# Optimization experiments

Measured on AMD Instinct MI355X. Metric: run time of the kernel, lower is better.

## Reference

```python
import jax, jax.numpy as jnp
import numpy as np

C = 256          # hidden_channel
FFN = 1024       # ffn_channel
NCLS = 10
BS, N = 2, 2048  # batch, num_proposals
GRID = 180.0     # grid_size/out_size_factor
EPS_OT = 10.0
IPOT_ITERS = 100


def _ln(x, g, b, eps=1e-5):
    mu = jnp.mean(x, axis=-1, keepdims=True)
    var = jnp.var(x, axis=-1, keepdims=True)
    return (x - mu) * jax.lax.rsqrt(var + eps) * g + b


def setup_inputs() -> dict:
    key = jax.random.key(0)
    ks = jax.random.split(key, 32)
    s = 0.02
    inp = {
        "pts_query_feat": jax.random.normal(ks[0], (BS, C, N), jnp.float32),
        "pts_query_pos": jax.random.uniform(ks[1], (BS, N, 2), jnp.float32) * GRID,
        "img_query_feat": jax.random.normal(ks[2], (BS, C, N), jnp.float32),
        "img_query_pos": jax.random.uniform(ks[3], (BS, N, 2), jnp.float32) * GRID,
        "pts_cls": jax.random.normal(ks[4], (BS, NCLS, N), jnp.float32),
        "img_cls": jax.random.normal(ks[5], (BS, NCLS, N), jnp.float32),
        # pts/img 1x1-conv projections
        "Wp": jax.random.normal(ks[6], (C, C), jnp.float32) * s,
        "bp": jnp.zeros((C,), jnp.float32),
        "Wi": jax.random.normal(ks[7], (C, C), jnp.float32) * s,
        "bi": jnp.zeros((C,), jnp.float32),
        # learned position embeddings (2 -> C)
        "Wqp": jax.random.normal(ks[8], (C, 2), jnp.float32) * s,
        "bqp": jnp.zeros((C,), jnp.float32),
        "Wkp": jax.random.normal(ks[9], (C, 2), jnp.float32) * s,
        "bkp": jnp.zeros((C,), jnp.float32),
        # out_projection: Linear(2C, C) + LayerNorm(C)
        "Wout": jax.random.normal(ks[10], (C, 2 * C), jnp.float32) * s,
        "bout": jnp.zeros((C,), jnp.float32),
        "g_out": jnp.ones((C,), jnp.float32),
        "beta_out": jnp.zeros((C,), jnp.float32),
        # ffn
        "Wf1": jax.random.normal(ks[11], (FFN, C), jnp.float32) * s,
        "bf1": jnp.zeros((FFN,), jnp.float32),
        "Wf2": jax.random.normal(ks[12], (C, FFN), jnp.float32) * s,
        "bf2": jnp.zeros((C,), jnp.float32),
        # final LayerNorm
        "g_ln": jnp.ones((C,), jnp.float32),
        "b_ln": jnp.zeros((C,), jnp.float32),
        # prediction head: 1x1 conv C -> 2 (center)
        "Wpred": jax.random.normal(ks[13], (2, C), jnp.float32) * s,
        "bpred": jnp.zeros((2,), jnp.float32),
    }
    return inp


def ipot(pts_feat, img_feat, pts_cls, img_cls, cost):
    # pts_feat/img_feat: [bs, C, N]; pts_cls/img_cls: [bs, N]; cost: [bs, N, N]
    n = pts_cls.shape[1]
    b0 = jnp.ones_like(pts_cls) / n
    G = jnp.exp(-cost / EPS_OT)
    res0 = jnp.ones_like(G)

    def step(carry, _):
        b, res = carry
        Q = jnp.maximum(G * res, 1e-6)
        a = pts_cls / (jnp.einsum("bnm,bm->bn", Q, b) + 1e-6)
        b = img_cls / (jnp.einsum("bnm,bn->bm", Q, a) + 1e-6)
        # diag_embed(a) @ Q @ diag_embed(b) == a[:,:,None] * Q * b[:,None,:]
        res = a[:, :, None] * Q * b[:, None, :]
        return (b, res), None

    (b, res), _ = jax.lax.scan(step, (b0, res0), None, length=IPOT_ITERS)
    # F.normalize(res, dim=2, p=1); res is nonnegative
    res = res / jnp.maximum(jnp.sum(jnp.abs(res), axis=2, keepdims=True), 1e-12)
    img_att = jnp.einsum("bnm,bcm->bcn", res, img_feat)  # [bs, C, N]
    return jnp.concatenate([pts_feat, img_att], axis=1)   # [bs, 2C, N]


def reference(pts_query_feat, pts_query_pos, img_query_feat, img_query_pos,
              pts_cls, img_cls,
              Wp, bp, Wi, bi, Wqp, bqp, Wkp, bkp,
              Wout, bout, g_out, beta_out,
              Wf1, bf1, Wf2, bf2, g_ln, b_ln, Wpred, bpred):
    # channel projections (1x1 conv over N)
    pf = jnp.einsum("oc,bcn->bon", Wp, pts_query_feat) + bp[:, None]
    imf = jnp.einsum("oc,bcn->bon", Wi, img_query_feat) + bi[:, None]
    # learned positional embeddings: [bs,N,2] -> [bs,C,N]
    pf = pf + jnp.einsum("cd,bnd->bcn", Wqp, pts_query_pos) + bqp[:, None]
    imf = imf + jnp.einsum("cd,bnd->bcn", Wkp, img_query_pos) + bkp[:, None]
    # detached per-proposal confidences
    pcls = jax.lax.stop_gradient(jnp.max(jax.nn.sigmoid(pts_cls), axis=1))
    icls = jax.lax.stop_gradient(jnp.max(jax.nn.sigmoid(img_cls), axis=1))
    # pairwise L2 cost [bs, N, N]
    diff = pts_query_pos[:, :, None, :] - img_query_pos[:, None, :, :]
    cost = jnp.sqrt(jnp.sum(diff * diff, axis=-1))
    feat = ipot(pf, imf, pcls, icls, cost)            # [bs, 2C, N]
    x = jnp.swapaxes(feat, 1, 2)                      # [bs, N, 2C]
    x = _ln(x @ Wout.T + bout, g_out, beta_out)       # out_projection
    ffn = jax.nn.relu(x @ Wf1.T + bf1) @ Wf2.T + bf2  # ffn
    x = ffn + x                                       # ffn(x) + dropout(x), eval mode
    x = jnp.swapaxes(_ln(x, g_ln, b_ln), 1, 2)        # [bs, C, N]
    center = jnp.einsum("oc,bcn->bon", Wpred, x) + bpred[:, None]
    center = center + jnp.swapaxes(pts_query_pos, 1, 2)  # [bs, 2, N]
    new_pos = jnp.swapaxes(jax.lax.stop_gradient(center), 1, 2)  # [bs, N, 2]
    return (x, new_pos, center)
```

## Files before the change

### kernel.cpp

```cpp
#include <hip/hip_runtime.h>
#include <hip/hip_bf16.h>

#define N2   2048
#define CH   256
#define FFNC 1024

typedef unsigned short ushort_t;
typedef unsigned int   uint_t;

#define OFF_QB     0u
#define OFF_IMFT   4194304u
#define OFF_CPART  5242880u
#define OFF_PCLS   7340032u
#define OFF_ICLS   7344128u
#define OFF_BVEC   7348224u
#define OFF_AVEC   7352320u
#define OFF_WOUTT  7356416u
#define OFF_WF1T   7487488u
#define OFF_WF2T   7749632u

__device__ __forceinline__ float bf2f(uint_t u) {
    return __uint_as_float(u << 16);
}
__device__ __forceinline__ ushort_t f2bf(float f) {
    __hip_bfloat16 h = __float2bfloat16(f);
    ushort_t u;
    __builtin_memcpy(&u, &h, 2);
    return u;
}

__device__ __forceinline__ void blockReduce2(float& x, float& y, float* sred) {
    #pragma unroll
    for (int off = 32; off; off >>= 1) {
        x += __shfl_xor(x, off);
        y += __shfl_xor(y, off);
    }
    const int wave = threadIdx.x >> 6, lane = threadIdx.x & 63;
    if (lane == 0) { sred[wave] = x; sred[4 + wave] = y; }
    __syncthreads();
    x = sred[0] + sred[1] + sred[2] + sred[3];
    y = sred[4] + sred[5] + sred[6] + sred[7];
    __syncthreads();
}

__global__ void __launch_bounds__(256) cls_max_k(
    const float* __restrict__ pc, const float* __restrict__ ic,
    float* __restrict__ pcls, float* __restrict__ icls) {
    const int g = blockIdx.x * 256 + threadIdx.x;
    const int b = g >> 11, n = g & 2047;
    float m1 = -1e30f, m2 = -1e30f;
    #pragma unroll
    for (int k = 0; k < 10; ++k) {
        const float v1 = pc[((size_t)b * 10 + k) * N2 + n];
        const float v2 = ic[((size_t)b * 10 + k) * N2 + n];
        m1 = fmaxf(m1, 1.f / (1.f + __expf(-v1)));
        m2 = fmaxf(m2, 1.f / (1.f + __expf(-v2)));
    }
    pcls[g] = m1; icls[g] = m2;
}

__global__ void __launch_bounds__(256) transpose_k(
    const float* __restrict__ in, float* __restrict__ out, int R, int C) {
    __shared__ float t[32][33];
    const int nct = C >> 5;
    const int bx = blockIdx.x % nct, by = blockIdx.x / nct;
    const int c0 = bx * 32, r0 = by * 32;
    const int tx = threadIdx.x & 31, ty = threadIdx.x >> 5;
    #pragma unroll
    for (int i = 0; i < 4; ++i) {
        const int r = ty + i * 8;
        t[r][tx] = in[(size_t)(r0 + r) * C + c0 + tx];
    }
    __syncthreads();
    #pragma unroll
    for (int i = 0; i < 4; ++i) {
        const int r = ty + i * 8;
        out[(size_t)(c0 + r) * R + r0 + tx] = t[tx][r];
    }
}

__global__ void __launch_bounds__(256) proj_rows(
    const float* __restrict__ F, const float* __restrict__ WT,
    const float* __restrict__ bias, const float* __restrict__ Wpos,
    const float* __restrict__ bpos, const float* __restrict__ pos,
    float* __restrict__ outb) {
    const int b = blockIdx.x >> 8;
    const int n0 = (blockIdx.x & 255) * 8;
    const int tid = threadIdx.x;
    __shared__ float s_x[8][256];
    for (int idx = tid; idx < 2048; idx += 256) {
        const int r = idx & 7, c = idx >> 3;
        s_x[r][c] = F[((size_t)b * CH + c) * N2 + n0 + r];
    }
    __syncthreads();
    float acc[8] = {0, 0, 0, 0, 0, 0, 0, 0};
    for (int c = 0; c < 256; ++c) {
        const float w = WT[(size_t)c * CH + tid];
        #pragma unroll
        for (int r = 0; r < 8; ++r) acc[r] += s_x[r][c] * w;
    }
    const float badd = bias[tid] + bpos[tid];
    const float w0 = Wpos[tid * 2 + 0], w1 = Wpos[tid * 2 + 1];
    #pragma unroll
    for (int r = 0; r < 8; ++r) {
        const int n = n0 + r;
        const float p0 = pos[((size_t)b * N2 + n) * 2 + 0];
        const float p1 = pos[((size_t)b * N2 + n) * 2 + 1];
        outb[((size_t)b * N2 + n) * CH + tid] = acc[r] + badd + w0 * p0 + w1 * p1;
    }
}


__device__ __forceinline__ void load_cols8(const float* ipos, int batch, int tid,
                                           float* ixr, float* iyr) {
    const float4* ip4 = (const float4*)(ipos + (size_t)batch * (N2 * 2));
    #pragma unroll
    for (int m = 0; m < 4; ++m) {
        const float4 v = ip4[4 * tid + m];
        ixr[2 * m + 0] = v.x; iyr[2 * m + 0] = v.y;
        ixr[2 * m + 1] = v.z; iyr[2 * m + 1] = v.w;
    }
}

__device__ __forceinline__ void unpack8(const uint4 v, float* q) {
    q[0] = bf2f(v.x & 0xffffu); q[1] = bf2f(v.x >> 16);
    q[2] = bf2f(v.y & 0xffffu); q[3] = bf2f(v.y >> 16);
    q[4] = bf2f(v.z & 0xffffu); q[5] = bf2f(v.z >> 16);
    q[6] = bf2f(v.w & 0xffffu); q[7] = bf2f(v.w >> 16);
}

__device__ __forceinline__ uint4 pack8(const float* q) {
    uint4 v;
    v.x = (uint_t)f2bf(q[0]) | ((uint_t)f2bf(q[1]) << 16);
    v.y = (uint_t)f2bf(q[2]) | ((uint_t)f2bf(q[3]) << 16);
    v.z = (uint_t)f2bf(q[4]) | ((uint_t)f2bf(q[5]) << 16);
    v.w = (uint_t)f2bf(q[6]) | ((uint_t)f2bf(q[7]) << 16);
    return v;
}

__global__ void __launch_bounds__(256, 4) ipot_init_k(
    ushort_t* __restrict__ Q, const float* __restrict__ ppos, const float* __restrict__ ipos,
    const float* __restrict__ pcls, float* __restrict__ avec, float* __restrict__ cpart) {
    const int blk = blockIdx.x;
    const int batch = blk >> 9;
    const int p = blk & 511;
    const int r0 = p * 4;
    const int tid = threadIdx.x, wave = tid >> 6, lane = tid & 63;
    __shared__ float s_tot[4][4];

    float ixr[8], iyr[8];
    load_cols8(ipos, batch, tid, ixr, iyr);
    float px[4], py[4], pcl4[4];
    #pragma unroll
    for (int j = 0; j < 4; ++j) {
        px[j] = ppos[((size_t)batch * N2 + r0 + j) * 2 + 0];
        py[j] = ppos[((size_t)batch * N2 + r0 + j) * 2 + 1];
        pcl4[j] = pcls[batch * N2 + r0 + j];
    }
    ushort_t* Qb = Q + (size_t)batch * N2 * N2;
    float cs[8] = {0, 0, 0, 0, 0, 0, 0, 0};

    float qn[4][8];
    float rd[4];
    #pragma unroll
    for (int jj = 0; jj < 4; ++jj) {
        rd[jj] = 0.f;
        #pragma unroll
        for (int k = 0; k < 8; ++k) {
            const float dx = px[jj] - ixr[k], dy = py[jj] - iyr[k];
            const float v = fmaxf(__expf(-0.1f * sqrtf(dx * dx + dy * dy)), 1e-6f);
            qn[jj][k] = bf2f(f2bf(v));
            rd[jj] += qn[jj][k];
        }
        ((uint4*)(Qb + (size_t)(r0 + jj) * N2))[tid] = pack8(qn[jj]);
    }
    #pragma unroll
    for (int off = 32; off; off >>= 1) {
        #pragma unroll
        for (int jj = 0; jj < 4; ++jj) rd[jj] += __shfl_xor(rd[jj], off);
    }
    if (lane == 0) {
        #pragma unroll
        for (int jj = 0; jj < 4; ++jj) s_tot[wave][jj] = rd[jj];
    }
    __syncthreads();
    #pragma unroll
    for (int jj = 0; jj < 4; ++jj) {
        const float tot = s_tot[0][jj] + s_tot[1][jj] + s_tot[2][jj] + s_tot[3][jj];
        const float a = pcl4[jj] / (tot * (1.f / 2048.f) + 1e-6f);
        if (tid == 0) avec[batch * N2 + r0 + jj] = a;
        #pragma unroll
        for (int k = 0; k < 8; ++k) cs[k] += a * qn[jj][k];
    }
    float4* cp4 = (float4*)(cpart + ((size_t)batch * 512 + p) * N2);
    float4 l, h4;
    l.x = cs[0]; l.y = cs[1]; l.z = cs[2]; l.w = cs[3];
    h4.x = cs[4]; h4.y = cs[5]; h4.z = cs[6]; h4.w = cs[7];
    cp4[2 * tid] = l; cp4[2 * tid + 1] = h4;
}

__global__ void __launch_bounds__(256) ipot_red_k(
    const float* __restrict__ cpart, const float* __restrict__ icls,
    float* __restrict__ bvec) {
    const int b = blockIdx.x >> 5;
    const int c0 = (blockIdx.x & 31) * 64;
    const int tid = threadIdx.x;
    const int c = tid & 63, pg = tid >> 6;
    __shared__ float s_part[4][64];
    const float* cpb = cpart + (size_t)b * 512 * N2 + c0 + c;
    float s = 0.f;
    #pragma unroll 8
    for (int k = 0; k < 128; ++k) s += cpb[(size_t)(pg + 4 * k) * N2];
    s_part[pg][c] = s;
    __syncthreads();
    if (tid < 64) {
        const float tot = s_part[0][tid] + s_part[1][tid] + s_part[2][tid] + s_part[3][tid];
        bvec[b * N2 + c0 + tid] = icls[b * N2 + c0 + tid] / (tot + 1e-6f);
    }
}

__global__ void __launch_bounds__(256, 4) ipot_ur_k(
    ushort_t* __restrict__ Q, const float* __restrict__ ppos, const float* __restrict__ ipos,
    const float* __restrict__ pcls, const float* __restrict__ bvec,
    float* __restrict__ avec, float* __restrict__ cpart) {
    const int blk = blockIdx.x;
    const int batch = blk >> 9;
    const int p = blk & 511;
    const int r0 = p * 4;
    const int tid = threadIdx.x, wave = tid >> 6, lane = tid & 63;
    __shared__ float s_tot[4][4];

    float ixr[8], iyr[8];
    load_cols8(ipos, batch, tid, ixr, iyr);
    float bb[8];
    {
        const float4* bv4 = (const float4*)(bvec + (size_t)batch * N2);
        const float4 l = bv4[2 * tid], h4 = bv4[2 * tid + 1];
        bb[0] = l.x; bb[1] = l.y; bb[2] = l.z; bb[3] = l.w;
        bb[4] = h4.x; bb[5] = h4.y; bb[6] = h4.z; bb[7] = h4.w;
    }
    float px[4], py[4], pcl4[4], a_cur[4];
    #pragma unroll
    for (int j = 0; j < 4; ++j) {
        px[j] = ppos[((size_t)batch * N2 + r0 + j) * 2 + 0];
        py[j] = ppos[((size_t)batch * N2 + r0 + j) * 2 + 1];
        pcl4[j] = pcls[batch * N2 + r0 + j];
        a_cur[j] = avec[batch * N2 + r0 + j];
    }
    ushort_t* Qb = Q + (size_t)batch * N2 * N2;
    float cs[8] = {0, 0, 0, 0, 0, 0, 0, 0};

    float qn[4][8];
    float rd[4];
    #pragma unroll
    for (int jj = 0; jj < 4; ++jj) {
        uint4* row4 = (uint4*)(Qb + (size_t)(r0 + jj) * N2);
        float qv[8];
        unpack8(row4[tid], qv);
        rd[jj] = 0.f;
        const float a = a_cur[jj];
        #pragma unroll
        for (int k = 0; k < 8; ++k) {
            const float dx = px[jj] - ixr[k], dy = py[jj] - iyr[k];
            const float G = __expf(-0.1f * sqrtf(dx * dx + dy * dy));
            const float v = fmaxf(G * ((a * qv[k]) * bb[k]), 1e-6f);
            qn[jj][k] = bf2f(f2bf(v));
            rd[jj] += qn[jj][k] * bb[k];
        }
        row4[tid] = pack8(qn[jj]);
    }
    #pragma unroll
    for (int off = 32; off; off >>= 1) {
        #pragma unroll
        for (int jj = 0; jj < 4; ++jj) rd[jj] += __shfl_xor(rd[jj], off);
    }
    if (lane == 0) {
        #pragma unroll
        for (int jj = 0; jj < 4; ++jj) s_tot[wave][jj] = rd[jj];
    }
    __syncthreads();
    #pragma unroll
    for (int jj = 0; jj < 4; ++jj) {
        const float tot = s_tot[0][jj] + s_tot[1][jj] + s_tot[2][jj] + s_tot[3][jj];
        const float a = pcl4[jj] / (tot + 1e-6f);
        if (tid == 0) avec[batch * N2 + r0 + jj] = a;
        #pragma unroll
        for (int k = 0; k < 8; ++k) cs[k] += a * qn[jj][k];
    }
    float4* cp4 = (float4*)(cpart + ((size_t)batch * 512 + p) * N2);
    float4 l, h4;
    l.x = cs[0]; l.y = cs[1]; l.z = cs[2]; l.w = cs[3];
    h4.x = cs[4]; h4.y = cs[5]; h4.z = cs[6]; h4.w = cs[7];
    cp4[2 * tid] = l; cp4[2 * tid + 1] = h4;
}

__global__ void __launch_bounds__(256, 4) ipot_fin_k(
    ushort_t* __restrict__ Q, const float* __restrict__ pcls,
    const float* __restrict__ bvec, const float* __restrict__ avec) {
    const int blk = blockIdx.x;
    const int batch = blk >> 9;
    const int p = blk & 511;
    const int r0 = p * 4;
    const int tid = threadIdx.x, wave = tid >> 6, lane = tid & 63;
    __shared__ float s_tot[4][4];

    float bb[8];
    {
        const float4* bv4 = (const float4*)(bvec + (size_t)batch * N2);
        const float4 l = bv4[2 * tid], h4 = bv4[2 * tid + 1];
        bb[0] = l.x; bb[1] = l.y; bb[2] = l.z; bb[3] = l.w;
        bb[4] = h4.x; bb[5] = h4.y; bb[6] = h4.z; bb[7] = h4.w;
    }
    float a4[4];
    #pragma unroll
    for (int j = 0; j < 4; ++j) a4[j] = avec[batch * N2 + r0 + j];
    ushort_t* Qb = Q + (size_t)batch * N2 * N2;

    float vv[4][8];
    float rs[4];
    #pragma unroll
    for (int jj = 0; jj < 4; ++jj) {
        uint4* row4 = (uint4*)(Qb + (size_t)(r0 + jj) * N2);
        float qv[8];
        unpack8(row4[tid], qv);
        rs[jj] = 0.f;
        const float a = a4[jj];
        #pragma unroll
        for (int k = 0; k < 8; ++k) {
            const float v = (a * qv[k]) * bb[k];
            vv[jj][k] = v;
            rs[jj] += v;
        }
    }
    #pragma unroll
    for (int off = 32; off; off >>= 1) {
        #pragma unroll
        for (int jj = 0; jj < 4; ++jj) rs[jj] += __shfl_xor(rs[jj], off);
    }
    if (lane == 0) {
        #pragma unroll
        for (int jj = 0; jj < 4; ++jj) s_tot[wave][jj] = rs[jj];
    }
    __syncthreads();
    #pragma unroll
    for (int jj = 0; jj < 4; ++jj) {
        const float tot = s_tot[0][jj] + s_tot[1][jj] + s_tot[2][jj] + s_tot[3][jj];
        const float sc = 1.f / fmaxf(tot, 1e-12f);
        float o[8];
        #pragma unroll
        for (int k = 0; k < 8; ++k) o[k] = vv[jj][k] * sc;
        ((uint4*)(Qb + (size_t)(r0 + jj) * N2))[tid] = pack8(o);
    }
}

__global__ void __launch_bounds__(256) att_zero_k(float* __restrict__ att) {
    const int idx = blockIdx.x * 256 + threadIdx.x;
    float4 z; z.x = 0.f; z.y = 0.f; z.z = 0.f; z.w = 0.f;
    ((float4*)att)[idx] = z;
}

__global__ void __launch_bounds__(256, 4) att_gemm(
    const ushort_t* __restrict__ R, const float* __restrict__ V, float* __restrict__ att) {
    const int bid = blockIdx.x;
    const int nt = bid & 31, ct = (bid >> 5) & 3, ks = (bid >> 7) & 3, b = bid >> 9;
    const int n0 = nt * 64, c0 = ct * 64, k00 = ks * 512;
    __shared__ float sRT[16][68];
    __shared__ float sV[16][68];
    const int tid = threadIdx.x;
    const int ny = tid & 15, cx = tid >> 4;
    float acc[4][4] = {};
    const ushort_t* Rb = R + (size_t)b * N2 * N2;
    const float* Vb = V + (size_t)b * N2 * CH;
    const int snl = tid & 63, skk0 = (tid >> 6) * 4;
    for (int k0 = k00; k0 < k00 + 512; k0 += 16) {
        {
            const uint2 v = *(const uint2*)&Rb[(size_t)(n0 + snl) * N2 + k0 + skk0];
            sRT[skk0 + 0][snl] = bf2f(v.x & 0xffffu);
            sRT[skk0 + 1][snl] = bf2f(v.x >> 16);
            sRT[skk0 + 2][snl] = bf2f(v.y & 0xffffu);
            sRT[skk0 + 3][snl] = bf2f(v.y >> 16);
        }
        for (int idx = tid; idx < 1024; idx += 256) {
            const int kk = idx >> 6, cl = idx & 63;
            sV[kk][cl] = Vb[(size_t)(k0 + kk) * CH + c0 + cl];
        }
        __syncthreads();
        #pragma unroll
        for (int kk = 0; kk < 16; ++kk) {
            const float4 av = *(const float4*)&sRT[kk][4 * ny];
            const float4 bv = *(const float4*)&sV[kk][4 * cx];
            acc[0][0] += av.x * bv.x; acc[0][1] += av.x * bv.y; acc[0][2] += av.x * bv.z; acc[0][3] += av.x * bv.w;
            acc[1][0] += av.y * bv.x; acc[1][1] += av.y * bv.y; acc[1][2] += av.y * bv.z; acc[1][3] += av.y * bv.w;
            acc[2][0] += av.z * bv.x; acc[2][1] += av.z * bv.y; acc[2][2] += av.z * bv.z; acc[2][3] += av.z * bv.w;
            acc[3][0] += av.w * bv.x; acc[3][1] += av.w * bv.y; acc[3][2] += av.w * bv.z; acc[3][3] += av.w * bv.w;
        }
        __syncthreads();
    }
    #pragma unroll
    for (int i = 0; i < 4; ++i)
        #pragma unroll
        for (int j = 0; j < 4; ++j)
            atomicAdd(&att[((size_t)b * N2 + n0 + 4 * ny + i) * CH + c0 + 4 * cx + j], acc[i][j]);
}

__global__ void __launch_bounds__(256) outproj_k(
    const float* __restrict__ pf, const float* __restrict__ att,
    const float* __restrict__ WoutT,
    const float* __restrict__ bout, const float* __restrict__ g,
    const float* __restrict__ be, float* __restrict__ y) {
    const int b = blockIdx.x >> 8;
    const int n0 = (blockIdx.x & 255) * 8;
    const int tid = threadIdx.x;
    __shared__ float s_x[8][512];
    __shared__ float sred[8];
    for (int idx = tid; idx < 2048; idx += 256) {
        const int k = idx & 255, r = idx >> 8;
        s_x[r][k] = pf[((size_t)b * N2 + n0 + r) * CH + k];
        s_x[r][256 + k] = att[((size_t)b * N2 + n0 + r) * CH + k];
    }
    __syncthreads();
    float acc[8] = {0, 0, 0, 0, 0, 0, 0, 0};
    for (int k = 0; k < 512; ++k) {
        const float w = WoutT[(size_t)k * CH + tid];
        #pragma unroll
        for (int r = 0; r < 8; ++r) acc[r] += s_x[r][k] * w;
    }
    const float bo = bout[tid], gg = g[tid], bb = be[tid];
    #pragma unroll
    for (int r = 0; r < 8; ++r) {
        const float v = acc[r] + bo;
        float s1 = v, s2 = v * v;
        blockReduce2(s1, s2, sred);
        const float mu = s1 * (1.f / 256.f);
        const float var = s2 * (1.f / 256.f) - mu * mu;
        y[((size_t)b * N2 + n0 + r) * CH + tid] = (v - mu) * rsqrtf(var + 1e-5f) * gg + bb;
    }
}

__global__ void __launch_bounds__(256) ffn_k(
    const float* __restrict__ y, const float* __restrict__ Wf1T,
    const float* __restrict__ bf1, const float* __restrict__ Wf2T,
    const float* __restrict__ bf2, const float* __restrict__ gln,
    const float* __restrict__ bln, const float* __restrict__ Wpred,
    const float* __restrict__ bpred, const float* __restrict__ pos,
    float* __restrict__ y2, float* __restrict__ out1,
    float* __restrict__ out2) {
    const int b = blockIdx.x >> 8;
    const int n0 = (blockIdx.x & 255) * 8;
    const int tid = threadIdx.x;
    __shared__ float s_y[8][256];
    __shared__ float s_h[8][1024];
    __shared__ float sred[8];
    for (int idx = tid; idx < 2048; idx += 256) {
        const int c = idx & 255, r = idx >> 8;
        s_y[r][c] = y[((size_t)b * N2 + n0 + r) * CH + c];
    }
    __syncthreads();
    float acc[4][8] = {};
    for (int c = 0; c < 256; ++c) {
        float yv[8];
        #pragma unroll
        for (int r = 0; r < 8; ++r) yv[r] = s_y[r][c];
        #pragma unroll
        for (int fi = 0; fi < 4; ++fi) {
            const float w = Wf1T[(size_t)c * FFNC + fi * 256 + tid];
            #pragma unroll
            for (int r = 0; r < 8; ++r) acc[fi][r] += yv[r] * w;
        }
    }
    #pragma unroll
    for (int fi = 0; fi < 4; ++fi) {
        const int f = fi * 256 + tid;
        const float bb = bf1[f];
        #pragma unroll
        for (int r = 0; r < 8; ++r) s_h[r][f] = fmaxf(acc[fi][r] + bb, 0.f);
    }
    __syncthreads();
    float a2[8] = {0, 0, 0, 0, 0, 0, 0, 0};
    for (int f = 0; f < 1024; ++f) {
        const float w = Wf2T[(size_t)f * CH + tid];
        #pragma unroll
        for (int r = 0; r < 8; ++r) a2[r] += s_h[r][f] * w;
    }
    const float bfv = bf2[tid], gg = gln[tid], bb2 = bln[tid];
    const float wp0 = Wpred[tid], wp1 = Wpred[CH + tid];
    #pragma unroll
    for (int r = 0; r < 8; ++r) {
        const int n = n0 + r;
        const float v = a2[r] + bfv + s_y[r][tid];
        float s1 = v, s2 = v * v;
        blockReduce2(s1, s2, sred);
        const float mu = s1 * (1.f / 256.f);
        const float var = s2 * (1.f / 256.f) - mu * mu;
        const float xo = (v - mu) * rsqrtf(var + 1e-5f) * gg + bb2;
        y2[((size_t)b * N2 + n) * CH + tid] = xo;
        float d0 = wp0 * xo, d1 = wp1 * xo;
        blockReduce2(d0, d1, sred);
        if (tid == 0) {
            const float c0v = d0 + bpred[0] + pos[((size_t)b * N2 + n) * 2 + 0];
            const float c1v = d1 + bpred[1] + pos[((size_t)b * N2 + n) * 2 + 1];
            out2[((size_t)b * 2 + 0) * N2 + n] = c0v;
            out2[((size_t)b * 2 + 1) * N2 + n] = c1v;
            out1[((size_t)b * N2 + n) * 2 + 0] = c0v;
            out1[((size_t)b * N2 + n) * 2 + 1] = c1v;
        }
    }
}

__global__ void __launch_bounds__(256) out_x_k(
    const float* __restrict__ y2, float* __restrict__ out0) {
    __shared__ float t[32][33];
    const int bid = blockIdx.x;
    const int ct = bid & 7, nt = (bid >> 3) & 63, b = bid >> 9;
    const int tx = threadIdx.x & 31, ty = threadIdx.x >> 5;
    #pragma unroll
    for (int i = 0; i < 4; ++i) {
        const int r = ty + i * 8;
        t[r][tx] = y2[((size_t)b * N2 + nt * 32 + r) * CH + ct * 32 + tx];
    }
    __syncthreads();
    #pragma unroll
    for (int i = 0; i < 4; ++i) {
        const int r = ty + i * 8;
        out0[((size_t)b * CH + ct * 32 + r) * N2 + nt * 32 + tx] = t[tx][r];
    }
}

extern "C" void kernel_launch(void* const* d_in, const int* in_sizes, int n_in,
                              void* d_out, int out_size, void* d_ws, size_t ws_size,
                              hipStream_t stream) {
    const float* ptsf  = (const float*)d_in[0];
    const float* ppos  = (const float*)d_in[1];
    const float* imgf  = (const float*)d_in[2];
    const float* ipos  = (const float*)d_in[3];
    const float* pcin  = (const float*)d_in[4];
    const float* icin  = (const float*)d_in[5];
    const float* Wp    = (const float*)d_in[6];
    const float* bp    = (const float*)d_in[7];
    const float* Wi    = (const float*)d_in[8];
    const float* bi    = (const float*)d_in[9];
    const float* Wqp   = (const float*)d_in[10];
    const float* bqp   = (const float*)d_in[11];
    const float* Wkp   = (const float*)d_in[12];
    const float* bkp   = (const float*)d_in[13];
    const float* Wout  = (const float*)d_in[14];
    const float* bout  = (const float*)d_in[15];
    const float* gout  = (const float*)d_in[16];
    const float* beo   = (const float*)d_in[17];
    const float* Wf1   = (const float*)d_in[18];
    const float* bf1   = (const float*)d_in[19];
    const float* Wf2   = (const float*)d_in[20];
    const float* bf2   = (const float*)d_in[21];
    const float* gln   = (const float*)d_in[22];
    const float* bln   = (const float*)d_in[23];
    const float* Wpred = (const float*)d_in[24];
    const float* bpred = (const float*)d_in[25];

    float* ws    = (float*)d_ws;
    ushort_t* Qw = (ushort_t*)d_ws;
    float* imfT  = ws + OFF_IMFT;
    float* cpart = ws + OFF_CPART;
    float* att   = ws + OFF_CPART;
    float* WiT   = ws + OFF_CPART;
    float* pcls  = ws + OFF_PCLS;
    float* icls  = ws + OFF_ICLS;
    float* bvec  = ws + OFF_BVEC;
    float* avec  = ws + OFF_AVEC;
    float* WoutT = ws + OFF_WOUTT;
    float* Wf1T  = ws + OFF_WF1T;
    float* Wf2T  = ws + OFF_WF2T;
    float* pf    = ws + 0u;
    float* yb    = ws + 1048576u;
    float* y2    = ws + 2097152u;
    float* WpT   = ws + 3145728u;

    float* out0 = (float*)d_out;
    float* out1 = out0 + (size_t)2 * CH * N2;
    float* out2 = out1 + (size_t)2 * N2 * 2;

    cls_max_k<<<16, 256, 0, stream>>>(pcin, icin, pcls, icls);
    transpose_k<<<64, 256, 0, stream>>>(Wi, WiT, 256, 256);
    proj_rows<<<512, 256, 0, stream>>>(imgf, WiT, bi, Wkp, bkp, ipos, imfT);
    transpose_k<<<128, 256, 0, stream>>>(Wout, WoutT, 256, 512);
    transpose_k<<<256, 256, 0, stream>>>(Wf1, Wf1T, 1024, 256);
    transpose_k<<<256, 256, 0, stream>>>(Wf2, Wf2T, 256, 1024);

    ipot_init_k<<<1024, 256, 0, stream>>>(Qw, ppos, ipos, pcls, avec, cpart);
    for (int t = 1; t < 100; ++t) {
        ipot_red_k<<<64, 256, 0, stream>>>(cpart, icls, bvec);
        ipot_ur_k<<<1024, 256, 0, stream>>>(Qw, ppos, ipos, pcls, bvec, avec, cpart);
    }
    ipot_red_k<<<64, 256, 0, stream>>>(cpart, icls, bvec);
    ipot_fin_k<<<1024, 256, 0, stream>>>(Qw, pcls, bvec, avec);

    att_zero_k<<<1024, 256, 0, stream>>>(att);
    att_gemm<<<1024, 256, 0, stream>>>(Qw, imfT, att);

    transpose_k<<<64, 256, 0, stream>>>(Wp, WpT, 256, 256);
    proj_rows<<<512, 256, 0, stream>>>(ptsf, WpT, bp, Wqp, bqp, ppos, pf);
    outproj_k<<<512, 256, 0, stream>>>(pf, att, WoutT, bout, gout, beo, yb);
    ffn_k<<<512, 256, 0, stream>>>(yb, Wf1T, bf1, Wf2T, bf2, gln, bln,
                                   Wpred, bpred, ppos, y2, out1, out2);
    out_x_k<<<1024, 256, 0, stream>>>(y2, out0);
}
```

Before: 2.581 ms.

## Fuse IPOT column reduction into update kernel with inter-block flag barrier

Removes the separate column-reduction launch from each IPOT iteration. The first 256 blocks of the update kernel compute bvec and bump a global counter, while every block loads its Q tile and computes the G*a*q product before spinning on the flag. The partial-sum buffer is double-buffered so that reads and writes within an iteration do not collide. This cuts launch count roughly in half and overlaps Q loading with the reduction. The cost is a cross-block spin-wait that relies on the reducer blocks being scheduled, and a slow fallback path if the wait times out.

```diff
diff --git a/kernel.cpp b/kernel.cpp
--- a/kernel.cpp
+++ b/kernel.cpp
@@ -10,14 +10,16 @@
 
 #define OFF_QB     0u
 #define OFF_IMFT   4194304u
-#define OFF_CPART  5242880u
-#define OFF_PCLS   7340032u
-#define OFF_ICLS   7344128u
-#define OFF_BVEC   7348224u
-#define OFF_AVEC   7352320u
-#define OFF_WOUTT  7356416u
-#define OFF_WF1T   7487488u
-#define OFF_WF2T   7749632u
+#define OFF_CPART0 5242880u
+#define OFF_CPART1 7340032u
+#define OFF_PCLS   9437184u
+#define OFF_ICLS   9441280u
+#define OFF_BVEC   9445376u
+#define OFF_AVEC   9449472u
+#define OFF_FLAG   9453568u
+#define OFF_WOUTT  9457664u
+#define OFF_WF1T   9588736u
+#define OFF_WF2T   9850880u
 
 __device__ __forceinline__ float bf2f(uint_t u) {
     return __uint_as_float(u << 16);
@@ -140,7 +142,8 @@
 
 __global__ void __launch_bounds__(256, 4) ipot_init_k(
     ushort_t* __restrict__ Q, const float* __restrict__ ppos, const float* __restrict__ ipos,
-    const float* __restrict__ pcls, float* __restrict__ avec, float* __restrict__ cpart) {
+    const float* __restrict__ pcls, float* __restrict__ avec, float* __restrict__ cpartW,
+    uint_t* __restrict__ flag) {
     const int blk = blockIdx.x;
     const int batch = blk >> 9;
     const int p = blk & 511;
@@ -148,6 +151,9 @@
     const int tid = threadIdx.x, wave = tid >> 6, lane = tid & 63;
     __shared__ float s_tot[4][4];
 
+    if (blk == 0 && tid == 0)
+        __hip_atomic_store(flag, 0u, __ATOMIC_RELAXED, __HIP_MEMORY_SCOPE_AGENT);
+
     float ixr[8], iyr[8];
     load_cols8(ipos, batch, tid, ixr, iyr);
     float px[4], py[4], pcl4[4];
@@ -192,7 +198,7 @@
         #pragma unroll
         for (int k = 0; k < 8; ++k) cs[k] += a * qn[jj][k];
     }
-    float4* cp4 = (float4*)(cpart + ((size_t)batch * 512 + p) * N2);
+    float4* cp4 = (float4*)(cpartW + ((size_t)batch * 512 + p) * N2);
     float4 l, h4;
     l.x = cs[0]; l.y = cs[1]; l.z = cs[2]; l.w = cs[3];
     h4.x = cs[4]; h4.y = cs[5]; h4.z = cs[6]; h4.w = cs[7];
@@ -221,24 +227,46 @@
 
 __global__ void __launch_bounds__(256, 4) ipot_ur_k(
     ushort_t* __restrict__ Q, const float* __restrict__ ppos, const float* __restrict__ ipos,
-    const float* __restrict__ pcls, const float* __restrict__ bvec,
-    float* __restrict__ avec, float* __restrict__ cpart) {
+    const float* __restrict__ pcls, const float* __restrict__ icls,
+    float* __restrict__ avec, const float* __restrict__ cpartR,
+    float* __restrict__ cpartW, float* __restrict__ bvec,
+    uint_t* __restrict__ flag, int t) {
     const int blk = blockIdx.x;
     const int batch = blk >> 9;
     const int p = blk & 511;
     const int r0 = p * 4;
     const int tid = threadIdx.x, wave = tid >> 6, lane = tid & 63;
     __shared__ float s_tot[4][4];
+    __shared__ float s_red[16][17];
+    __shared__ int s_fb;
+
+    if (blk < 256) {
+        const int pb = blk >> 7;
+        const int c0 = (blk & 127) * 16;
+        const int cl = tid & 15, pg = tid >> 4;
+        const float* cpb = cpartR + (size_t)pb * 512 * N2 + c0 + cl;
+        float s = 0.f;
+        #pragma unroll 8
+        for (int k = 0; k < 32; ++k) s += cpb[(size_t)(pg + 16 * k) * N2];
+        s_red[pg][cl] = s;
+        __syncthreads();
+        if (tid < 16) {
+            float tot = 0.f;
+            #pragma unroll
+            for (int g2 = 0; g2 < 16; ++g2) tot += s_red[g2][tid];
+            const float bv = icls[pb * N2 + c0 + tid] / (tot + 1e-6f);
+            __hip_atomic_store(&bvec[pb * N2 + c0 + tid], bv,
+                               __ATOMIC_RELAXED, __HIP_MEMORY_SCOPE_AGENT);
+        }
+        __syncthreads();
+        if (tid == 0) {
+            __threadfence();
+            __hip_atomic_fetch_add(flag, 1u, __ATOMIC_RELEASE, __HIP_MEMORY_SCOPE_AGENT);
+        }
+    }
 
     float ixr[8], iyr[8];
     load_cols8(ipos, batch, tid, ixr, iyr);
-    float bb[8];
-    {
-        const float4* bv4 = (const float4*)(bvec + (size_t)batch * N2);
-        const float4 l = bv4[2 * tid], h4 = bv4[2 * tid + 1];
-        bb[0] = l.x; bb[1] = l.y; bb[2] = l.z; bb[3] = l.w;
-        bb[4] = h4.x; bb[5] = h4.y; bb[6] = h4.z; bb[7] = h4.w;
-    }
     float px[4], py[4], pcl4[4], a_cur[4];
     #pragma unroll
     for (int j = 0; j < 4; ++j) {
@@ -248,26 +276,61 @@
         a_cur[j] = avec[batch * N2 + r0 + j];
     }
     ushort_t* Qb = Q + (size_t)batch * N2 * N2;
-    float cs[8] = {0, 0, 0, 0, 0, 0, 0, 0};
-
-    float qn[4][8];
-    float rd[4];
+    float w[4][8];
     #pragma unroll
     for (int jj = 0; jj < 4; ++jj) {
-        uint4* row4 = (uint4*)(Qb + (size_t)(r0 + jj) * N2);
         float qv[8];
-        unpack8(row4[tid], qv);
-        rd[jj] = 0.f;
+        unpack8(((const uint4*)(Qb + (size_t)(r0 + jj) * N2))[tid], qv);
         const float a = a_cur[jj];
         #pragma unroll
         for (int k = 0; k < 8; ++k) {
             const float dx = px[jj] - ixr[k], dy = py[jj] - iyr[k];
             const float G = __expf(-0.1f * sqrtf(dx * dx + dy * dy));
-            const float v = fmaxf(G * ((a * qv[k]) * bb[k]), 1e-6f);
+            w[jj][k] = G * (a * qv[k]);
+        }
+    }
+
+    if (tid == 0) {
+        s_fb = 0;
+        const uint_t target = 256u * (uint_t)t;
+        int spins = 0;
+        while (__hip_atomic_load(flag, __ATOMIC_ACQUIRE, __HIP_MEMORY_SCOPE_AGENT) < target) {
+            __builtin_amdgcn_s_sleep(8);
+            if (++spins > 50000) { s_fb = 1; break; }
+        }
+    }
+    __syncthreads();
+
+    float bb[8];
+    if (s_fb) {
+        #pragma unroll
+        for (int k = 0; k < 8; ++k) {
+            const int col = 8 * tid + k;
+            float s = 0.f;
+            for (int pp = 0; pp < 512; ++pp)
+                s += cpartR[(size_t)batch * 512 * N2 + (size_t)pp * N2 + col];
+            bb[k] = icls[batch * N2 + col] / (s + 1e-6f);
+        }
+    } else {
+        const float* bvb = bvec + (size_t)batch * N2 + 8 * tid;
+        #pragma unroll
+        for (int k = 0; k < 8; ++k)
+            bb[k] = __hip_atomic_load(&bvb[k], __ATOMIC_RELAXED, __HIP_MEMORY_SCOPE_AGENT);
+    }
+
+    float cs[8] = {0, 0, 0, 0, 0, 0, 0, 0};
+    float qn[4][8];
+    float rd[4];
+    #pragma unroll
+    for (int jj = 0; jj < 4; ++jj) {
+        rd[jj] = 0.f;
+        #pragma unroll
+        for (int k = 0; k < 8; ++k) {
+            const float v = fmaxf(w[jj][k] * bb[k], 1e-6f);
             qn[jj][k] = bf2f(f2bf(v));
             rd[jj] += qn[jj][k] * bb[k];
         }
-        row4[tid] = pack8(qn[jj]);
+        ((uint4*)(Qb + (size_t)(r0 + jj) * N2))[tid] = pack8(qn[jj]);
     }
     #pragma unroll
     for (int off = 32; off; off >>= 1) {
@@ -287,7 +350,7 @@
         #pragma unroll
         for (int k = 0; k < 8; ++k) cs[k] += a * qn[jj][k];
     }
-    float4* cp4 = (float4*)(cpart + ((size_t)batch * 512 + p) * N2);
+    float4* cp4 = (float4*)(cpartW + ((size_t)batch * 512 + p) * N2);
     float4 l, h4;
     l.x = cs[0]; l.y = cs[1]; l.z = cs[2]; l.w = cs[3];
     h4.x = cs[4]; h4.y = cs[5]; h4.z = cs[6]; h4.w = cs[7];
@@ -320,9 +383,8 @@
     float rs[4];
     #pragma unroll
     for (int jj = 0; jj < 4; ++jj) {
-        uint4* row4 = (uint4*)(Qb + (size_t)(r0 + jj) * N2);
         float qv[8];
-        unpack8(row4[tid], qv);
+        unpack8(((const uint4*)(Qb + (size_t)(r0 + jj) * N2))[tid], qv);
         rs[jj] = 0.f;
         const float a = a4[jj];
         #pragma unroll
@@ -556,23 +618,25 @@
     const float* Wpred = (const float*)d_in[24];
     const float* bpred = (const float*)d_in[25];
 
-    float* ws    = (float*)d_ws;
-    ushort_t* Qw = (ushort_t*)d_ws;
-    float* imfT  = ws + OFF_IMFT;
-    float* cpart = ws + OFF_CPART;
-    float* att   = ws + OFF_CPART;
-    float* WiT   = ws + OFF_CPART;
-    float* pcls  = ws + OFF_PCLS;
-    float* icls  = ws + OFF_ICLS;
-    float* bvec  = ws + OFF_BVEC;
-    float* avec  = ws + OFF_AVEC;
-    float* WoutT = ws + OFF_WOUTT;
-    float* Wf1T  = ws + OFF_WF1T;
-    float* Wf2T  = ws + OFF_WF2T;
-    float* pf    = ws + 0u;
-    float* yb    = ws + 1048576u;
-    float* y2    = ws + 2097152u;
-    float* WpT   = ws + 3145728u;
+    float* ws     = (float*)d_ws;
+    ushort_t* Qw  = (ushort_t*)d_ws;
+    float* imfT   = ws + OFF_IMFT;
+    float* cpart0 = ws + OFF_CPART0;
+    float* cpart1 = ws + OFF_CPART1;
+    float* att    = ws + OFF_CPART0;
+    float* WiT    = ws + OFF_CPART0;
+    float* pcls   = ws + OFF_PCLS;
+    float* icls   = ws + OFF_ICLS;
+    float* bvec   = ws + OFF_BVEC;
+    float* avec   = ws + OFF_AVEC;
+    uint_t* flag  = (uint_t*)(ws + OFF_FLAG);
+    float* WoutT  = ws + OFF_WOUTT;
+    float* Wf1T   = ws + OFF_WF1T;
+    float* Wf2T   = ws + OFF_WF2T;
+    float* pf     = ws + 0u;
+    float* yb     = ws + 1048576u;
+    float* y2     = ws + 2097152u;
+    float* WpT    = ws + 3145728u;
 
     float* out0 = (float*)d_out;
     float* out1 = out0 + (size_t)2 * CH * N2;
@@ -585,12 +649,14 @@
     transpose_k<<<256, 256, 0, stream>>>(Wf1, Wf1T, 1024, 256);
     transpose_k<<<256, 256, 0, stream>>>(Wf2, Wf2T, 256, 1024);
 
-    ipot_init_k<<<1024, 256, 0, stream>>>(Qw, ppos, ipos, pcls, avec, cpart);
+    ipot_init_k<<<1024, 256, 0, stream>>>(Qw, ppos, ipos, pcls, avec, cpart1, flag);
     for (int t = 1; t < 100; ++t) {
-        ipot_red_k<<<64, 256, 0, stream>>>(cpart, icls, bvec);
-        ipot_ur_k<<<1024, 256, 0, stream>>>(Qw, ppos, ipos, pcls, bvec, avec, cpart);
-    }
-    ipot_red_k<<<64, 256, 0, stream>>>(cpart, icls, bvec);
+        float* cR = (t & 1) ? cpart1 : cpart0;
+        float* cW = (t & 1) ? cpart0 : cpart1;
+        ipot_ur_k<<<1024, 256, 0, stream>>>(Qw, ppos, ipos, pcls, icls, avec,
+                                            cR, cW, bvec, flag, t);
+    }
+    ipot_red_k<<<64, 256, 0, stream>>>(cpart0, icls, bvec);
     ipot_fin_k<<<1024, 256, 0, stream>>>(Qw, pcls, bvec, avec);
 
     att_zero_k<<<1024, 256, 0, stream>>>(att);
```

New measurement: 8.787 ms. 3.4x slower.
